# Kernel tuning notes

Hardware: AMD Instinct MI355X
Metric: run time of the kernel (lower is better)

## Reference

```python
import jax, jax.numpy as jnp
import numpy as np

N = 50000      # nodes
E = 800000     # edges
F_IN = 64      # num_node_features
H = 128        # hidden_channels
C = 2          # num_classes
G = 16         # graphs in batch


def setup_inputs() -> dict:
    key = jax.random.key(0)
    ks = jax.random.split(key, 16)
    def lin(k, fan_in, shape):
        return jax.random.normal(k, shape, jnp.float32) / np.sqrt(fan_in)
    return {
        "x": jax.random.normal(ks[0], (N, F_IN), jnp.float32),
        "edge_index": jax.random.randint(ks[1], (2, E), 0, N, dtype=jnp.int32),
        "batch": jnp.sort(jax.random.randint(ks[2], (N,), 0, G, dtype=jnp.int32)),
        "W1": lin(ks[3], F_IN, (F_IN, H)), "b1": jnp.zeros((H,), jnp.float32),
        "W2": lin(ks[4], H, (H, H)),       "b2": jnp.zeros((H,), jnp.float32),
        "W3": lin(ks[5], H, (H, H)),       "b3": jnp.zeros((H,), jnp.float32),
        "W4": lin(ks[6], H, (H, H)),       "b4": jnp.zeros((H,), jnp.float32),
        "lw1": lin(ks[7], H, (H, H // 2)), "lb1": jnp.zeros((H // 2,), jnp.float32),
        "lw2": lin(ks[8], H // 2, (H // 2, C)), "lb2": jnp.zeros((C,), jnp.float32),
    }


def _graph_norm(edge_index):
    # PyG GCNConv default: add self-loops, symmetric normalization.
    loop = jnp.arange(N, dtype=edge_index.dtype)
    src = jnp.concatenate([edge_index[0], loop])  # message source
    dst = jnp.concatenate([edge_index[1], loop])  # aggregation target
    deg = jax.ops.segment_sum(jnp.ones_like(dst, jnp.float32), dst, num_segments=N)
    dinv = jnp.where(deg > 0, jax.lax.rsqrt(deg), 0.0)
    norm = dinv[src] * dinv[dst]                  # [E+N]
    return src, dst, norm


def _gcn_conv(h, W, b, src, dst, norm):
    hw = h @ W                                    # [N, out]
    msg = hw[src] * norm[:, None]                 # gather + normalize  [E+N, out]
    agg = jax.ops.segment_sum(msg, dst, num_segments=N)  # scatter-add
    return agg + b


def reference(x, edge_index, batch, W1, b1, W2, b2, W3, b3, W4, b4, lw1, lb1, lw2, lb2):
    src, dst, norm = _graph_norm(edge_index)
    h = jax.nn.relu(_gcn_conv(x, W1, b1, src, dst, norm))   # dropout inactive (eval)
    h = jax.nn.relu(_gcn_conv(h, W2, b2, src, dst, norm))
    h = jax.nn.relu(_gcn_conv(h, W3, b3, src, dst, norm))
    h = _gcn_conv(h, W4, b4, src, dst, norm)
    # global_mean_pool over graph ids
    cnt = jax.ops.segment_sum(jnp.ones((N,), jnp.float32), batch, num_segments=G)
    pooled = jax.ops.segment_sum(h, batch, num_segments=G) / jnp.maximum(cnt, 1.0)[:, None]
    out = jax.nn.relu(pooled @ lw1 + lb1)
    return out @ lw2 + lb2
```

## Files before the change

kernel.cpp:

```cpp
#include <hip/hip_runtime.h>

#define NN 50000
#define NPAD 50048
#define NE 800000
#define FIN 64
#define H 128
#define NG 16
#define POOL_BLOCKS 1000
#define POOL_NODES 50
#define NPART 64
#define NBUCK 98
#define BUCK_CAP 10000
#define FILLA_BLOCKS 512
#define FILLA_CHUNK 1563
#define CHUNK_U 16
#define DUMMY NN
#define AGG_CH (NN / 16)
#define PREP_ITEMS (NPAD * FIN + H * FIN + 3 * H * H)
#define PREP_BLOCKS ((PREP_ITEMS + 255) / 256)

typedef __bf16 bf16x8 __attribute__((ext_vector_type(8)));
typedef float f32x4 __attribute__((ext_vector_type(4)));

__device__ inline unsigned short bf16r(float x) {
    unsigned int u = __float_as_uint(x);
    return (unsigned short)((u + 0x7fffu + ((u >> 16) & 1u)) >> 16);
}
__device__ inline unsigned int pack_bf16x2(float a, float b) {
    return (unsigned int)bf16r(a) | ((unsigned int)bf16r(b) << 16);
}
__device__ inline float bf_lo(unsigned int u) { return __uint_as_float(u << 16); }
__device__ inline float bf_hi(unsigned int u) { return __uint_as_float(u & 0xffff0000u); }

__global__ __launch_bounds__(256) void fillA_prep_kernel(const int* __restrict__ ei,
                                                         int* __restrict__ gcount,
                                                         unsigned int* __restrict__ ebuf,
                                                         const float* __restrict__ x,
                                                         const float* __restrict__ W1,
                                                         const float* __restrict__ W2,
                                                         const float* __restrict__ W3,
                                                         const float* __restrict__ W4,
                                                         unsigned short* __restrict__ xb,
                                                         unsigned short* __restrict__ Wt1,
                                                         unsigned short* __restrict__ Wt2,
                                                         unsigned short* __restrict__ Wt3,
                                                         unsigned short* __restrict__ Wt4) {
    const int t = threadIdx.x;
    if (blockIdx.x >= FILLA_BLOCKS) {
        int e = (blockIdx.x - FILLA_BLOCKS) * 256 + t;
        if (e < NPAD * FIN) {
            int n = e >> 6, k = e & 63;
            unsigned short v = (n < NN) ? bf16r(x[n * FIN + k]) : (unsigned short)0;
            xb[(size_t)(k >> 5) * (NPAD * 32) + n * 32 + (k & 31)] = v;
            return;
        }
        int tt = e - NPAD * FIN;
        if (tt < H * FIN) {
            int n = tt / FIN, k = tt % FIN;
            Wt1[tt] = bf16r(W1[k * H + n]);
            return;
        }
        int u = tt - H * FIN;
        const float* W = W2;
        unsigned short* Wt = Wt2;
        if (u >= 2 * H * H) { W = W4; Wt = Wt4; u -= 2 * H * H; }
        else if (u >= H * H) { W = W3; Wt = Wt3; u -= H * H; }
        if (u < H * H) {
            int n = u / H, k = u % H;
            Wt[u] = bf16r(W[k * H + n]);
        }
        return;
    }
    __shared__ int hist[128];
    __shared__ int base[128];
    if (t < 128) hist[t] = 0;
    __syncthreads();
    const int e0 = blockIdx.x * FILLA_CHUNK;
    const int e1 = min(e0 + FILLA_CHUNK, NE);
    for (int e = e0 + t; e < e1; e += 256)
        atomicAdd(&hist[ei[NE + e] >> 9], 1);
    __syncthreads();
    if (t < 128) {
        int h = (t < NBUCK) ? hist[t] : 0;
        base[t] = h ? atomicAdd(&gcount[t], h) : 0;
    }
    __syncthreads();
    for (int e = e0 + t; e < e1; e += 256) {
        int d = ei[NE + e];
        int s = ei[e];
        int b = d >> 9;
        int pos = atomicAdd(&base[b], 1);
        ebuf[b * BUCK_CAP + pos] = (unsigned int)s | ((unsigned int)d << 16);
    }
}

__global__ __launch_bounds__(256) void fillB_kernel(const unsigned int* __restrict__ ebuf,
                                                    const int* __restrict__ gcount,
                                                    int* __restrict__ galloc,
                                                    int2* __restrict__ rowse,
                                                    float* __restrict__ dinv,
                                                    unsigned short* __restrict__ csr) {
    __shared__ int lh[512];
    __shared__ int lsum[256];
    __shared__ int loff[512];
    __shared__ int lcur[512];
    __shared__ int base_s;
    const int b = blockIdx.x, t = threadIdx.x;
    const int n0 = b * 512;
    lh[t] = 0;
    lh[t + 256] = 0;
    __syncthreads();
    const int ne = gcount[b];
    const unsigned int* __restrict__ eb = ebuf + b * BUCK_CAP;
    for (int i = t; i < ne; i += 256)
        atomicAdd(&lh[(int)(eb[i] >> 16) - n0], 1);
    __syncthreads();
    const int c0 = lh[2 * t], c1 = lh[2 * t + 1];
    const int p0 = (c0 + 7) & ~7, p1 = (c1 + 7) & ~7;
    lsum[t] = p0 + p1;
    __syncthreads();
    for (int off = 1; off < 256; off <<= 1) {
        int u = (t >= off) ? lsum[t - off] : 0;
        __syncthreads();
        lsum[t] += u;
        __syncthreads();
    }
    if (t == 255) base_s = atomicAdd(galloc, lsum[255]);
    int excl = (t == 0) ? 0 : lsum[t - 1];
    __syncthreads();
    const int base = base_s;
    loff[2 * t] = excl;
    loff[2 * t + 1] = excl + p0;
    {
        int j = 2 * t, n = n0 + j;
        int st = base + excl;
        if (n < NN) {
            rowse[n] = make_int2(st, st + p0);
            dinv[n] = rsqrtf((float)c0 + 1.0f);
        } else if (n < NPAD) {
            rowse[n] = make_int2(0, 0);
            dinv[n] = 0.0f;
        }
        lcur[j] = st;
        int st1 = st + p0, n1 = n + 1;
        if (n1 < NN) {
            rowse[n1] = make_int2(st1, st1 + p1);
            dinv[n1] = rsqrtf((float)c1 + 1.0f);
        } else if (n1 < NPAD) {
            rowse[n1] = make_int2(0, 0);
            dinv[n1] = 0.0f;
        }
        lcur[j + 1] = st1;
    }
    __syncthreads();
    for (int i = t; i < ne; i += 256) {
        unsigned int u = eb[i];
        int s = (int)(u & 0xFFFFu);
        int j = (int)(u >> 16) - n0;
        int pos = atomicAdd(&lcur[j], 1);
        csr[pos] = (unsigned short)s;
    }
    __syncthreads();
    {
        int j = 2 * t;
        int st = base + loff[j] + c0, en = base + loff[j] + p0;
        for (int k = st; k < en; k++) csr[k] = (unsigned short)DUMMY;
        int st1 = base + loff[j + 1] + c1, en1 = base + loff[j + 1] + p1;
        for (int k = st1; k < en1; k++) csr[k] = (unsigned short)DUMMY;
    }
}

#define LSTRIDE 130
template <int K>
__global__ __launch_bounds__(256) void gemm_mfma_kernel(const unsigned short* __restrict__ hb,
                                                        const unsigned short* __restrict__ Wt,
                                                        const float* __restrict__ dinv,
                                                        unsigned int* __restrict__ outu) {
    __shared__ float ls[64 * LSTRIDE];
    const int wave = threadIdx.x >> 6, lane = threadIdx.x & 63;
    const int m15 = lane & 15, quad = lane >> 4;
    const int row0 = blockIdx.x * 64;
    const int arow = row0 + wave * 16 + m15;

    bf16x8 a[K / 32];
#pragma unroll
    for (int ks = 0; ks < K / 32; ks++)
        a[ks] = *(const bf16x8*)&hb[(size_t)ks * (NPAD * 32) + arow * 32 + quad * 8];

    const int lrow = wave * 16 + quad * 4;
    float dv[4];
#pragma unroll
    for (int r = 0; r < 4; r++) dv[r] = dinv[row0 + lrow + r];

#pragma unroll
    for (int ct = 0; ct < 8; ct++) {
        f32x4 acc = {0.f, 0.f, 0.f, 0.f};
#pragma unroll
        for (int ks = 0; ks < K / 32; ks++) {
            bf16x8 b = *(const bf16x8*)&Wt[(ct * 16 + m15) * K + ks * 32 + quad * 8];
            acc = __builtin_amdgcn_mfma_f32_16x16x32_bf16(a[ks], b, acc, 0, 0, 0);
        }
#pragma unroll
        for (int r = 0; r < 4; r++)
            ls[(lrow + r) * LSTRIDE + ct * 16 + m15] = acc[r] * dv[r];
    }
    __syncthreads();

#pragma unroll
    for (int k = 0; k < 4; k++) {
        int idx = threadIdx.x + 256 * k;
        int c = idx >> 8, row = (idx >> 2) & 63, q = idx & 3;
        const float* p = &ls[row * LSTRIDE + c * 32 + q * 8];
        uint4 o;
        o.x = pack_bf16x2(p[0], p[1]);
        o.y = pack_bf16x2(p[2], p[3]);
        o.z = pack_bf16x2(p[4], p[5]);
        o.w = pack_bf16x2(p[6], p[7]);
        *(uint4*)&outu[(size_t)c * (NPAD * CHUNK_U) + (size_t)(row0 + row) * CHUNK_U + q * 4] = o;
    }
}

template <bool RELU_BIAS>
__global__ __launch_bounds__(256) void agg_kernel(const unsigned int* __restrict__ hwc,
                                                  const int2* __restrict__ rowse,
                                                  const unsigned short* __restrict__ csr,
                                                  const float* __restrict__ dinv,
                                                  const float* __restrict__ bias,
                                                  unsigned int* __restrict__ outc) {
    const int chunk = blockIdx.x / AGG_CH;
    const int nb = blockIdx.x % AGG_CH;
    const int wave = threadIdx.x >> 6, lane = threadIdx.x & 63;
    const int g = lane >> 4, u = lane & 15;
    const int n = nb * 16 + wave * 4 + g;
    const unsigned int* __restrict__ slice = hwc + (size_t)chunk * (NPAD * CHUNK_U);

    unsigned int sv = slice[n * CHUNK_U + u];
    float ax = bf_lo(sv), ay = bf_hi(sv);

    const int2 se = rowse[n];
    for (int i = se.x; i < se.y; i += 8) {
        uint4 c = *(const uint4*)&csr[i];
        int s0 = c.x & 0xFFFF, s1 = c.x >> 16;
        int s2 = c.y & 0xFFFF, s3 = c.y >> 16;
        int s4 = c.z & 0xFFFF, s5 = c.z >> 16;
        int s6 = c.w & 0xFFFF, s7 = c.w >> 16;
        unsigned int v0 = slice[s0 * CHUNK_U + u], v1 = slice[s1 * CHUNK_U + u];
        unsigned int v2 = slice[s2 * CHUNK_U + u], v3 = slice[s3 * CHUNK_U + u];
        unsigned int v4 = slice[s4 * CHUNK_U + u], v5 = slice[s5 * CHUNK_U + u];
        unsigned int v6 = slice[s6 * CHUNK_U + u], v7 = slice[s7 * CHUNK_U + u];
        ax += bf_lo(v0) + bf_lo(v1) + bf_lo(v2) + bf_lo(v3) +
              bf_lo(v4) + bf_lo(v5) + bf_lo(v6) + bf_lo(v7);
        ay += bf_hi(v0) + bf_hi(v1) + bf_hi(v2) + bf_hi(v3) +
              bf_hi(v4) + bf_hi(v5) + bf_hi(v6) + bf_hi(v7);
    }

    float d = dinv[n];
    ax *= d;
    ay *= d;
    if (RELU_BIAS) {
        float2 bv = ((const float2*)bias)[chunk * CHUNK_U + u];
        ax = fmaxf(ax + bv.x, 0.f);
        ay = fmaxf(ay + bv.y, 0.f);
    }
    outc[(size_t)chunk * (NPAD * CHUNK_U) + n * CHUNK_U + u] = pack_bf16x2(ax, ay);
}

__global__ __launch_bounds__(256) void pool_kernel(const unsigned int* __restrict__ hbu,
                                                   const float* __restrict__ b4,
                                                   const int* __restrict__ batch,
                                                   float* __restrict__ poolpart,
                                                   float* __restrict__ pcntpart) {
    __shared__ int bs[POOL_NODES];
    const int tid = threadIdx.x;
    const int n0 = blockIdx.x * POOL_NODES;
    if (tid < POOL_NODES) bs[tid] = batch[n0 + tid];
    __syncthreads();
    float* __restrict__ pooled = poolpart + (blockIdx.x & (NPART - 1)) * (NG * H);
    float* __restrict__ cnt = pcntpart + (blockIdx.x & (NPART - 1)) * NG;
    const int c2 = tid & 63;
    const int chunk = c2 >> 4, u = c2 & 15;
    const int rsub = tid >> 6;
    float2 bb = ((const float2*)b4)[c2];
    float2 acc = {0.f, 0.f};
    float cacc = 0.f;
    int curg = bs[rsub];
    const size_t coff = (size_t)chunk * (NPAD * CHUNK_U) + u;
    for (int r = rsub; r < POOL_NODES; r += 4) {
        int g = bs[r];
        if (g != curg) {
            atomicAdd(&pooled[curg * H + c2 * 2], acc.x);
            atomicAdd(&pooled[curg * H + c2 * 2 + 1], acc.y);
            if (c2 == 0) atomicAdd(&cnt[curg], cacc);
            acc.x = acc.y = 0.f;
            cacc = 0.f;
            curg = g;
        }
        unsigned int v = hbu[coff + (size_t)(n0 + r) * CHUNK_U];
        acc.x += bf_lo(v) + bb.x;
        acc.y += bf_hi(v) + bb.y;
        cacc += 1.f;
    }
    atomicAdd(&pooled[curg * H + c2 * 2], acc.x);
    atomicAdd(&pooled[curg * H + c2 * 2 + 1], acc.y);
    if (c2 == 0) atomicAdd(&cnt[curg], cacc);
}

__global__ __launch_bounds__(1024) void mlp_kernel(const float* __restrict__ poolpart,
                                                   const float* __restrict__ pcntpart,
                                                   const float* __restrict__ lw1,
                                                   const float* __restrict__ lb1,
                                                   const float* __restrict__ lw2,
                                                   const float* __restrict__ lb2,
                                                   float* __restrict__ out) {
    __shared__ float mean_s[NG * H];
    __shared__ float cnt_s[NG];
    __shared__ float hid_s[NG * 64];
    int tid = threadIdx.x;
    if (tid < NG) {
        float c = 0.f;
        for (int p = 0; p < NPART; p++) c += pcntpart[p * NG + tid];
        cnt_s[tid] = fmaxf(c, 1.0f);
    }
    __syncthreads();
    for (int i = tid; i < NG * H; i += 1024) {
        float s = 0.f;
        for (int p = 0; p < NPART; p++) s += poolpart[p * (NG * H) + i];
        mean_s[i] = s / cnt_s[i >> 7];
    }
    __syncthreads();
    {
        int g = tid >> 6, j = tid & 63;
        float acc = lb1[j];
        for (int f = 0; f < H; f++) acc += mean_s[g * H + f] * lw1[f * 64 + j];
        hid_s[g * 64 + j] = fmaxf(acc, 0.f);
    }
    __syncthreads();
    if (tid < 32) {
        int g = tid >> 1, c = tid & 1;
        float acc = lb2[c];
        for (int j = 0; j < 64; j++) acc += hid_s[g * 64 + j] * lw2[j * 2 + c];
        out[g * 2 + c] = acc;
    }
}

extern "C" void kernel_launch(void* const* d_in, const int* in_sizes, int n_in,
                              void* d_out, int out_size, void* d_ws, size_t ws_size,
                              hipStream_t stream) {
    const float* x = (const float*)d_in[0];
    const int* ei = (const int*)d_in[1];
    const int* batch = (const int*)d_in[2];
    const float* W1 = (const float*)d_in[3];
    const float* b1 = (const float*)d_in[4];
    const float* W2 = (const float*)d_in[5];
    const float* b2 = (const float*)d_in[6];
    const float* W3 = (const float*)d_in[7];
    const float* b3 = (const float*)d_in[8];
    const float* W4 = (const float*)d_in[9];
    const float* b4 = (const float*)d_in[10];
    const float* lw1 = (const float*)d_in[11];
    const float* lb1 = (const float*)d_in[12];
    const float* lw2 = (const float*)d_in[13];
    const float* lb2 = (const float*)d_in[14];
    float* out = (float*)d_out;

    int* wsi = (int*)d_ws;
    int* gcount = wsi;
    int* galloc = wsi + 128;
    float* poolpart = (float*)(wsi + 256);
    float* pcntpart = (float*)(wsi + 131328);
    int2* rowse = (int2*)(wsi + 132352);
    unsigned short* csr = (unsigned short*)(wsi + 232448);
    float* dinv = (float*)(wsi + 832448);
    unsigned short* Wt1 = (unsigned short*)(wsi + 882496);
    unsigned short* Wt2 = (unsigned short*)(wsi + 886592);
    unsigned short* Wt3 = (unsigned short*)(wsi + 894784);
    unsigned short* Wt4 = (unsigned short*)(wsi + 902976);
    unsigned short* xb = (unsigned short*)(wsi + 911168);
    unsigned int* hb = (unsigned int*)(wsi + 2512704);
    unsigned int* hwb = (unsigned int*)(wsi + 5715776);
    unsigned int* ebuf = (unsigned int*)(wsi + 8918848);

    const int gemmBlocks = NPAD / 64;
    const int aggBlocks = 4 * AGG_CH;

    hipMemsetAsync(wsi, 0, 132352 * sizeof(int), stream);
    fillA_prep_kernel<<<FILLA_BLOCKS + PREP_BLOCKS, 256, 0, stream>>>(
        ei, gcount, ebuf, x, W1, W2, W3, W4, xb, Wt1, Wt2, Wt3, Wt4);
    fillB_kernel<<<NBUCK, 256, 0, stream>>>(ebuf, gcount, galloc, rowse, dinv, csr);

    gemm_mfma_kernel<FIN><<<gemmBlocks, 256, 0, stream>>>(xb, Wt1, dinv, hwb);
    agg_kernel<true><<<aggBlocks, 256, 0, stream>>>(hwb, rowse, csr, dinv, b1, hb);
    gemm_mfma_kernel<H><<<gemmBlocks, 256, 0, stream>>>((unsigned short*)hb, Wt2, dinv, hwb);
    agg_kernel<true><<<aggBlocks, 256, 0, stream>>>(hwb, rowse, csr, dinv, b2, hb);
    gemm_mfma_kernel<H><<<gemmBlocks, 256, 0, stream>>>((unsigned short*)hb, Wt3, dinv, hwb);
    agg_kernel<true><<<aggBlocks, 256, 0, stream>>>(hwb, rowse, csr, dinv, b3, hb);
    gemm_mfma_kernel<H><<<gemmBlocks, 256, 0, stream>>>((unsigned short*)hb, Wt4, dinv, hwb);
    agg_kernel<false><<<aggBlocks, 256, 0, stream>>>(hwb, rowse, csr, dinv, nullptr, hb);

    pool_kernel<<<POOL_BLOCKS, 256, 0, stream>>>(hb, b4, batch, poolpart, pcntpart);
    mlp_kernel<<<1, 1024, 0, stream>>>(poolpart, pcntpart, lw1, lb1, lw2, lb2, out);
}
```

Baseline: 346.4 us.

## Vectorize aggregation per thread, double CSR buckets, move pool zeroing into prep

The aggregation kernel now gives each thread four packed bf16 words (a uint4) per node instead of one word, and accumulates with packed f32 adds. This cuts the number of threads and per-edge index loads and issues wider gathers. The CSR build uses 196 buckets of 256 nodes instead of 98 of 512, so fillB runs with more blocks and less serial work per thread. Zeroing of the pool partial buffers moves from the memset into the prep kernel, leaving a much smaller memset. The cost is less thread-level parallelism in the latency-bound gather.

```diff
diff --git a/kernel.cpp b/kernel.cpp
--- a/kernel.cpp
+++ b/kernel.cpp
@@ -9,18 +9,20 @@
 #define POOL_BLOCKS 1000
 #define POOL_NODES 50
 #define NPART 64
-#define NBUCK 98
-#define BUCK_CAP 10000
+#define NBUCK 196
+#define BUCK_CAP 4800
 #define FILLA_BLOCKS 512
 #define FILLA_CHUNK 1563
 #define CHUNK_U 16
 #define DUMMY NN
-#define AGG_CH (NN / 16)
-#define PREP_ITEMS (NPAD * FIN + H * FIN + 3 * H * H)
+#define AGG_CH (NPAD / 64)
+#define ZERO_I4 33024
+#define PREP_ITEMS (NPAD * FIN + H * FIN + 3 * H * H + ZERO_I4)
 #define PREP_BLOCKS ((PREP_ITEMS + 255) / 256)
 
 typedef __bf16 bf16x8 __attribute__((ext_vector_type(8)));
 typedef float f32x4 __attribute__((ext_vector_type(4)));
+typedef float f32x2 __attribute__((ext_vector_type(2)));
 
 __device__ inline unsigned short bf16r(float x) {
     unsigned int u = __float_as_uint(x);
@@ -31,6 +33,13 @@
 }
 __device__ inline float bf_lo(unsigned int u) { return __uint_as_float(u << 16); }
 __device__ inline float bf_hi(unsigned int u) { return __uint_as_float(u & 0xffff0000u); }
+
+__device__ inline void pkadd(f32x2& a, unsigned int u) {
+    f32x2 p;
+    p.x = bf_lo(u);
+    p.y = bf_hi(u);
+    asm("v_pk_add_f32 %0, %1, %0" : "+v"(a) : "v"(p));
+}
 
 __global__ __launch_bounds__(256) void fillA_prep_kernel(const int* __restrict__ ei,
                                                          int* __restrict__ gcount,
@@ -44,7 +53,8 @@
                                                          unsigned short* __restrict__ Wt1,
                                                          unsigned short* __restrict__ Wt2,
                                                          unsigned short* __restrict__ Wt3,
-                                                         unsigned short* __restrict__ Wt4) {
+                                                         unsigned short* __restrict__ Wt4,
+                                                         int4* __restrict__ zbuf) {
     const int t = threadIdx.x;
     if (blockIdx.x >= FILLA_BLOCKS) {
         int e = (blockIdx.x - FILLA_BLOCKS) * 256 + t;
@@ -61,34 +71,37 @@
             return;
         }
         int u = tt - H * FIN;
-        const float* W = W2;
-        unsigned short* Wt = Wt2;
-        if (u >= 2 * H * H) { W = W4; Wt = Wt4; u -= 2 * H * H; }
-        else if (u >= H * H) { W = W3; Wt = Wt3; u -= H * H; }
-        if (u < H * H) {
+        if (u < 3 * H * H) {
+            const float* W = W2;
+            unsigned short* Wt = Wt2;
+            if (u >= 2 * H * H) { W = W4; Wt = Wt4; u -= 2 * H * H; }
+            else if (u >= H * H) { W = W3; Wt = Wt3; u -= H * H; }
             int n = u / H, k = u % H;
             Wt[u] = bf16r(W[k * H + n]);
+            return;
         }
+        int z = u - 3 * H * H;
+        if (z < ZERO_I4) zbuf[z] = make_int4(0, 0, 0, 0);
         return;
     }
-    __shared__ int hist[128];
-    __shared__ int base[128];
-    if (t < 128) hist[t] = 0;
+    __shared__ int hist[256];
+    __shared__ int base[256];
+    hist[t] = 0;
     __syncthreads();
     const int e0 = blockIdx.x * FILLA_CHUNK;
     const int e1 = min(e0 + FILLA_CHUNK, NE);
     for (int e = e0 + t; e < e1; e += 256)
-        atomicAdd(&hist[ei[NE + e] >> 9], 1);
-    __syncthreads();
-    if (t < 128) {
-        int h = (t < NBUCK) ? hist[t] : 0;
+        atomicAdd(&hist[ei[NE + e] >> 8], 1);
+    __syncthreads();
+    {
+        int h = hist[t];
         base[t] = h ? atomicAdd(&gcount[t], h) : 0;
     }
     __syncthreads();
     for (int e = e0 + t; e < e1; e += 256) {
         int d = ei[NE + e];
         int s = ei[e];
-        int b = d >> 9;
+        int b = d >> 8;
         int pos = atomicAdd(&base[b], 1);
         ebuf[b * BUCK_CAP + pos] = (unsigned int)s | ((unsigned int)d << 16);
     }
@@ -100,24 +113,22 @@
                                                     int2* __restrict__ rowse,
                                                     float* __restrict__ dinv,
                                                     unsigned short* __restrict__ csr) {
-    __shared__ int lh[512];
+    __shared__ int lh[256];
     __shared__ int lsum[256];
-    __shared__ int loff[512];
-    __shared__ int lcur[512];
+    __shared__ int lcur[256];
     __shared__ int base_s;
     const int b = blockIdx.x, t = threadIdx.x;
-    const int n0 = b * 512;
+    const int n0 = b * 256;
     lh[t] = 0;
-    lh[t + 256] = 0;
     __syncthreads();
     const int ne = gcount[b];
     const unsigned int* __restrict__ eb = ebuf + b * BUCK_CAP;
     for (int i = t; i < ne; i += 256)
         atomicAdd(&lh[(int)(eb[i] >> 16) - n0], 1);
     __syncthreads();
-    const int c0 = lh[2 * t], c1 = lh[2 * t + 1];
-    const int p0 = (c0 + 7) & ~7, p1 = (c1 + 7) & ~7;
-    lsum[t] = p0 + p1;
+    const int c = lh[t];
+    const int p = (c + 7) & ~7;
+    lsum[t] = p;
     __syncthreads();
     for (int off = 1; off < 256; off <<= 1) {
         int u = (t >= off) ? lsum[t - off] : 0;
@@ -126,48 +137,26 @@
         __syncthreads();
     }
     if (t == 255) base_s = atomicAdd(galloc, lsum[255]);
-    int excl = (t == 0) ? 0 : lsum[t - 1];
-    __syncthreads();
-    const int base = base_s;
-    loff[2 * t] = excl;
-    loff[2 * t + 1] = excl + p0;
-    {
-        int j = 2 * t, n = n0 + j;
-        int st = base + excl;
-        if (n < NN) {
-            rowse[n] = make_int2(st, st + p0);
-            dinv[n] = rsqrtf((float)c0 + 1.0f);
-        } else if (n < NPAD) {
-            rowse[n] = make_int2(0, 0);
-            dinv[n] = 0.0f;
-        }
-        lcur[j] = st;
-        int st1 = st + p0, n1 = n + 1;
-        if (n1 < NN) {
-            rowse[n1] = make_int2(st1, st1 + p1);
-            dinv[n1] = rsqrtf((float)c1 + 1.0f);
-        } else if (n1 < NPAD) {
-            rowse[n1] = make_int2(0, 0);
-            dinv[n1] = 0.0f;
-        }
-        lcur[j + 1] = st1;
-    }
+    const int excl = t ? lsum[t - 1] : 0;
+    __syncthreads();
+    const int st = base_s + excl;
+    const int n = n0 + t;
+    if (n < NN) {
+        rowse[n] = make_int2(st, st + p);
+        dinv[n] = rsqrtf((float)c + 1.0f);
+    } else if (n < NPAD) {
+        rowse[n] = make_int2(0, 0);
+        dinv[n] = 0.0f;
+    }
+    lcur[t] = st;
     __syncthreads();
     for (int i = t; i < ne; i += 256) {
         unsigned int u = eb[i];
-        int s = (int)(u & 0xFFFFu);
-        int j = (int)(u >> 16) - n0;
-        int pos = atomicAdd(&lcur[j], 1);
-        csr[pos] = (unsigned short)s;
-    }
-    __syncthreads();
-    {
-        int j = 2 * t;
-        int st = base + loff[j] + c0, en = base + loff[j] + p0;
-        for (int k = st; k < en; k++) csr[k] = (unsigned short)DUMMY;
-        int st1 = base + loff[j + 1] + c1, en1 = base + loff[j + 1] + p1;
-        for (int k = st1; k < en1; k++) csr[k] = (unsigned short)DUMMY;
-    }
+        int pos = atomicAdd(&lcur[(int)(u >> 16) - n0], 1);
+        csr[pos] = (unsigned short)(u & 0xFFFFu);
+    }
+    __syncthreads();
+    for (int k = st + c; k < st + p; k++) csr[k] = (unsigned short)DUMMY;
 }
 
 #define LSTRIDE 130
@@ -229,13 +218,16 @@
                                                   unsigned int* __restrict__ outc) {
     const int chunk = blockIdx.x / AGG_CH;
     const int nb = blockIdx.x % AGG_CH;
-    const int wave = threadIdx.x >> 6, lane = threadIdx.x & 63;
-    const int g = lane >> 4, u = lane & 15;
-    const int n = nb * 16 + wave * 4 + g;
+    const int g = threadIdx.x & 3;
+    const int n = nb * 64 + (threadIdx.x >> 2);
+    const int u0 = g * 4;
     const unsigned int* __restrict__ slice = hwc + (size_t)chunk * (NPAD * CHUNK_U);
 
-    unsigned int sv = slice[n * CHUNK_U + u];
-    float ax = bf_lo(sv), ay = bf_hi(sv);
+    uint4 sv = *(const uint4*)&slice[n * CHUNK_U + u0];
+    f32x2 a0 = {bf_lo(sv.x), bf_hi(sv.x)};
+    f32x2 a1 = {bf_lo(sv.y), bf_hi(sv.y)};
+    f32x2 a2 = {bf_lo(sv.z), bf_hi(sv.z)};
+    f32x2 a3 = {bf_lo(sv.w), bf_hi(sv.w)};
 
     const int2 se = rowse[n];
     for (int i = se.x; i < se.y; i += 8) {
@@ -244,25 +236,40 @@
         int s2 = c.y & 0xFFFF, s3 = c.y >> 16;
         int s4 = c.z & 0xFFFF, s5 = c.z >> 16;
         int s6 = c.w & 0xFFFF, s7 = c.w >> 16;
-        unsigned int v0 = slice[s0 * CHUNK_U + u], v1 = slice[s1 * CHUNK_U + u];
-        unsigned int v2 = slice[s2 * CHUNK_U + u], v3 = slice[s3 * CHUNK_U + u];
-        unsigned int v4 = slice[s4 * CHUNK_U + u], v5 = slice[s5 * CHUNK_U + u];
-        unsigned int v6 = slice[s6 * CHUNK_U + u], v7 = slice[s7 * CHUNK_U + u];
-        ax += bf_lo(v0) + bf_lo(v1) + bf_lo(v2) + bf_lo(v3) +
-              bf_lo(v4) + bf_lo(v5) + bf_lo(v6) + bf_lo(v7);
-        ay += bf_hi(v0) + bf_hi(v1) + bf_hi(v2) + bf_hi(v3) +
-              bf_hi(v4) + bf_hi(v5) + bf_hi(v6) + bf_hi(v7);
-    }
-
-    float d = dinv[n];
-    ax *= d;
-    ay *= d;
+        uint4 v0 = *(const uint4*)&slice[s0 * CHUNK_U + u0];
+        uint4 v1 = *(const uint4*)&slice[s1 * CHUNK_U + u0];
+        uint4 v2 = *(const uint4*)&slice[s2 * CHUNK_U + u0];
+        uint4 v3 = *(const uint4*)&slice[s3 * CHUNK_U + u0];
+        uint4 v4 = *(const uint4*)&slice[s4 * CHUNK_U + u0];
+        uint4 v5 = *(const uint4*)&slice[s5 * CHUNK_U + u0];
+        uint4 v6 = *(const uint4*)&slice[s6 * CHUNK_U + u0];
+        uint4 v7 = *(const uint4*)&slice[s7 * CHUNK_U + u0];
+        pkadd(a0, v0.x); pkadd(a1, v0.y); pkadd(a2, v0.z); pkadd(a3, v0.w);
+        pkadd(a0, v1.x); pkadd(a1, v1.y); pkadd(a2, v1.z); pkadd(a3, v1.w);
+        pkadd(a0, v2.x); pkadd(a1, v2.y); pkadd(a2, v2.z); pkadd(a3, v2.w);
+        pkadd(a0, v3.x); pkadd(a1, v3.y); pkadd(a2, v3.z); pkadd(a3, v3.w);
+        pkadd(a0, v4.x); pkadd(a1, v4.y); pkadd(a2, v4.z); pkadd(a3, v4.w);
+        pkadd(a0, v5.x); pkadd(a1, v5.y); pkadd(a2, v5.z); pkadd(a3, v5.w);
+        pkadd(a0, v6.x); pkadd(a1, v6.y); pkadd(a2, v6.z); pkadd(a3, v6.w);
+        pkadd(a0, v7.x); pkadd(a1, v7.y); pkadd(a2, v7.z); pkadd(a3, v7.w);
+    }
+
+    const float d = dinv[n];
+    uint4 o;
     if (RELU_BIAS) {
-        float2 bv = ((const float2*)bias)[chunk * CHUNK_U + u];
-        ax = fmaxf(ax + bv.x, 0.f);
-        ay = fmaxf(ay + bv.y, 0.f);
-    }
-    outc[(size_t)chunk * (NPAD * CHUNK_U) + n * CHUNK_U + u] = pack_bf16x2(ax, ay);
+        const float2* bp = (const float2*)bias + chunk * CHUNK_U + u0;
+        float2 q0 = bp[0], q1 = bp[1], q2 = bp[2], q3 = bp[3];
+        o.x = pack_bf16x2(fmaxf(a0.x * d + q0.x, 0.f), fmaxf(a0.y * d + q0.y, 0.f));
+        o.y = pack_bf16x2(fmaxf(a1.x * d + q1.x, 0.f), fmaxf(a1.y * d + q1.y, 0.f));
+        o.z = pack_bf16x2(fmaxf(a2.x * d + q2.x, 0.f), fmaxf(a2.y * d + q2.y, 0.f));
+        o.w = pack_bf16x2(fmaxf(a3.x * d + q3.x, 0.f), fmaxf(a3.y * d + q3.y, 0.f));
+    } else {
+        o.x = pack_bf16x2(a0.x * d, a0.y * d);
+        o.y = pack_bf16x2(a1.x * d, a1.y * d);
+        o.z = pack_bf16x2(a2.x * d, a2.y * d);
+        o.w = pack_bf16x2(a3.x * d, a3.y * d);
+    }
+    *(uint4*)&outc[(size_t)chunk * (NPAD * CHUNK_U) + (size_t)n * CHUNK_U + u0] = o;
 }
 
 __global__ __launch_bounds__(256) void pool_kernel(const unsigned int* __restrict__ hbu,
@@ -365,27 +372,27 @@
 
     int* wsi = (int*)d_ws;
     int* gcount = wsi;
-    int* galloc = wsi + 128;
-    float* poolpart = (float*)(wsi + 256);
-    float* pcntpart = (float*)(wsi + 131328);
-    int2* rowse = (int2*)(wsi + 132352);
-    unsigned short* csr = (unsigned short*)(wsi + 232448);
-    float* dinv = (float*)(wsi + 832448);
-    unsigned short* Wt1 = (unsigned short*)(wsi + 882496);
-    unsigned short* Wt2 = (unsigned short*)(wsi + 886592);
-    unsigned short* Wt3 = (unsigned short*)(wsi + 894784);
-    unsigned short* Wt4 = (unsigned short*)(wsi + 902976);
-    unsigned short* xb = (unsigned short*)(wsi + 911168);
-    unsigned int* hb = (unsigned int*)(wsi + 2512704);
-    unsigned int* hwb = (unsigned int*)(wsi + 5715776);
-    unsigned int* ebuf = (unsigned int*)(wsi + 8918848);
+    int* galloc = wsi + 256;
+    float* poolpart = (float*)(wsi + 512);
+    float* pcntpart = (float*)(wsi + 131584);
+    int2* rowse = (int2*)(wsi + 132608);
+    unsigned short* csr = (unsigned short*)(wsi + 232704);
+    float* dinv = (float*)(wsi + 832704);
+    unsigned short* Wt1 = (unsigned short*)(wsi + 882752);
+    unsigned short* Wt2 = (unsigned short*)(wsi + 886848);
+    unsigned short* Wt3 = (unsigned short*)(wsi + 895040);
+    unsigned short* Wt4 = (unsigned short*)(wsi + 903232);
+    unsigned short* xb = (unsigned short*)(wsi + 911424);
+    unsigned int* hb = (unsigned int*)(wsi + 2512960);
+    unsigned int* hwb = (unsigned int*)(wsi + 5716032);
+    unsigned int* ebuf = (unsigned int*)(wsi + 8919104);
 
     const int gemmBlocks = NPAD / 64;
     const int aggBlocks = 4 * AGG_CH;
 
-    hipMemsetAsync(wsi, 0, 132352 * sizeof(int), stream);
+    hipMemsetAsync(wsi, 0, 512 * sizeof(int), stream);
     fillA_prep_kernel<<<FILLA_BLOCKS + PREP_BLOCKS, 256, 0, stream>>>(
-        ei, gcount, ebuf, x, W1, W2, W3, W4, xb, Wt1, Wt2, Wt3, Wt4);
+        ei, gcount, ebuf, x, W1, W2, W3, W4, xb, Wt1, Wt2, Wt3, Wt4, (int4*)poolpart);
     fillB_kernel<<<NBUCK, 256, 0, stream>>>(ebuf, gcount, galloc, rowse, dinv, csr);
 
     gemm_mfma_kernel<FIN><<<gemmBlocks, 256, 0, stream>>>(xb, Wt1, dinv, hwb);
```

New measurement: 334.2 us. -3.5%, faster.
